# Kernel optimization log

Hardware: AMD Instinct MI355X
Metric: run time of the kernel (lower is better)

Reference implementation:

```python
import jax, jax.numpy as jnp
import numpy as np

B, S, H, E, I, K = 1, 4096, 1024, 16, 512, 2
ISH = 1024  # shared expert intermediate = moe_intermediate_size * num_shared_experts
ROUTE_SCALE = 1.0
WSCALE = 0.02


def setup_inputs() -> dict:
    key = jax.random.key(0)
    ks = jax.random.split(key, 9)
    return {
        "hidden_states": jax.random.normal(ks[0], (B, S, H), dtype=jnp.float32),
        "router_w": jax.random.normal(ks[1], (H, E), dtype=jnp.float32) * WSCALE,
        "expert_bias": jnp.zeros((E,), dtype=jnp.float32),
        "w_gate": jax.random.normal(ks[2], (E, H, I), dtype=jnp.float32) * WSCALE,
        "w_up": jax.random.normal(ks[3], (E, H, I), dtype=jnp.float32) * WSCALE,
        "w_down": jax.random.normal(ks[4], (E, I, H), dtype=jnp.float32) * WSCALE,
        "sw_gate": jax.random.normal(ks[5], (H, ISH), dtype=jnp.float32) * WSCALE,
        "sw_up": jax.random.normal(ks[6], (H, ISH), dtype=jnp.float32) * WSCALE,
        "sw_down": jax.random.normal(ks[7], (ISH, H), dtype=jnp.float32) * WSCALE,
    }


def reference(hidden_states, router_w, expert_bias, w_gate, w_up, w_down, sw_gate, sw_up, sw_down):
    b, s, h = hidden_states.shape
    T = b * s
    xf = hidden_states.reshape(T, h)

    # --- token-choice router (sigmoid scores, top-k, normalize, scale) ---
    scores = jax.nn.sigmoid((xf @ router_w).astype(jnp.float32))          # [T, E]
    _, sel = jax.lax.top_k(scores + expert_bias[None, :], K)              # [T, K] int32
    top = jnp.take_along_axis(scores, sel, axis=1)                        # [T, K]
    top = top / (top.sum(axis=-1, keepdims=True) + 1e-20)
    top = top * ROUTE_SCALE

    # combine weights: [T, E], zero for unselected experts
    comb = jnp.zeros((T, E), jnp.float32).at[jnp.arange(T)[:, None], sel].add(top)

    # --- routed experts: SwiGLU MLP per expert (stacked weights) ---
    g = jnp.einsum('th,ehi->eti', xf, w_gate)                             # [E, T, I]
    u = jnp.einsum('th,ehi->eti', xf, w_up)                               # [E, T, I]
    a = jax.nn.silu(g) * u                                                # [E, T, I]
    eo = jnp.einsum('eti,eih->eth', a, w_down)                            # [E, T, H]
    routed = jnp.einsum('eth,te->th', eo.astype(jnp.float32), comb).astype(hidden_states.dtype)

    # --- shared experts (always active) ---
    shared = (jax.nn.silu(xf @ sw_gate) * (xf @ sw_up)) @ sw_down         # [T, H]

    return (shared + routed).reshape(b, s, h)
```

## Files before the change

kernel.cpp:

```cpp
#include <hip/hip_runtime.h>
#include <math.h>

#define T_TOK 4096
#define HDIM  1024
#define NEXP  16
#define IDIM  512
#define NSLOT 16384
#define NGRP  18
#define MAXRB 160

typedef unsigned int u32;
typedef unsigned short u16;
typedef __attribute__((ext_vector_type(8))) short bfrag;
typedef __attribute__((ext_vector_type(4))) float f32x4;

__device__ __forceinline__ u16 f2bf(float f) {
    union { float f; u32 u; } c; c.f = f;
    u32 u = c.u;
    u32 r = u + 0x7fffu + ((u >> 16) & 1u);
    return (u16)(r >> 16);
}
__device__ __forceinline__ float bf2f(u16 h) {
    union { u32 u; float f; } c; c.u = ((u32)h) << 16;
    return c.f;
}

__device__ __forceinline__ void async16(void* lds, const void* g) {
    __builtin_amdgcn_global_load_lds((__attribute__((address_space(1))) void*)(g),
                                     (__attribute__((address_space(3))) void*)(lds),
                                     16, 0, 0);
}

#define SYNCN(n) do { \
    asm volatile("s_waitcnt vmcnt(" #n ")" ::: "memory"); \
    __builtin_amdgcn_s_barrier(); \
    __builtin_amdgcn_sched_barrier(0); \
} while (0)
#define BAR2() do { \
    __builtin_amdgcn_s_barrier(); \
    __builtin_amdgcn_sched_barrier(0); \
} while (0)

__global__ __launch_bounds__(256) void cvt_f32_bf16(const float* __restrict__ src,
                                                    u16* __restrict__ dst, int n) {
    int i = (blockIdx.x * 256 + threadIdx.x) * 4;
    if (i >= n) return;
    float4 v = *(const float4*)(src + i);
    ushort4 o;
    o.x = f2bf(v.x); o.y = f2bf(v.y); o.z = f2bf(v.z); o.w = f2bf(v.w);
    *(ushort4*)(dst + i) = o;
}

__global__ __launch_bounds__(256) void transpose_k(const float* __restrict__ src,
                                                   u16* __restrict__ dst,
                                                   int R, int C, long bstride) {
    __shared__ float tile[32][33];
    long base = (long)blockIdx.z * bstride;
    int c0 = blockIdx.x * 32, r0 = blockIdx.y * 32;
    int tx = threadIdx.x, ty = threadIdx.y;
#pragma unroll
    for (int j = 0; j < 4; ++j)
        tile[ty + 8 * j][tx] = src[base + (long)(r0 + ty + 8 * j) * C + (c0 + tx)];
    __syncthreads();
#pragma unroll
    for (int j = 0; j < 4; ++j)
        dst[base + (long)(c0 + ty + 8 * j) * R + (r0 + tx)] = f2bf(tile[tx][ty + 8 * j]);
}

__global__ __launch_bounds__(256) void router_k(const float* __restrict__ x,
                                                const float* __restrict__ rw,
                                                const float* __restrict__ bias,
                                                int* __restrict__ sel,
                                                float* __restrict__ wts) {
    int tid = threadIdx.x;
    int wv = tid >> 6;
    int lane = tid & 63;
    int t = blockIdx.x * 4 + wv;
    int e = lane & 15, hc = lane >> 4;
    const float* xr = x + (long)t * HDIM + hc * 256;
    const float* rp = rw + (long)hc * 256 * NEXP + e;
    float acc = 0.f;
#pragma unroll 4
    for (int i = 0; i < 64; ++i) {
        float4 xv = *(const float4*)(xr + i * 4);
        acc += xv.x * rp[(i * 4 + 0) * NEXP] + xv.y * rp[(i * 4 + 1) * NEXP]
             + xv.z * rp[(i * 4 + 2) * NEXP] + xv.w * rp[(i * 4 + 3) * NEXP];
    }
    acc += __shfl_down(acc, 16);
    acc += __shfl_down(acc, 32);
    float sc = 1.f / (1.f + __expf(-acc));
    float v = sc + bias[e];
    int i0 = -1, i1 = -1;
    float v0 = -1e30f, v1 = -1e30f, s0 = 0.f, s1 = 0.f;
#pragma unroll
    for (int j = 0; j < 16; ++j) {
        float vj = __shfl(v, j);
        float scj = __shfl(sc, j);
        if (vj > v0) { v1 = v0; i1 = i0; s1 = s0; v0 = vj; i0 = j; s0 = scj; }
        else if (vj > v1) { v1 = vj; i1 = j; s1 = scj; }
    }
    if (lane == 0) {
        float nrm = s0 + s1 + 1e-20f;
        sel[t * 2] = i0; sel[t * 2 + 1] = i1;
        wts[t * 2] = s0 / nrm; wts[t * 2 + 1] = s1 / nrm;
    }
}

__global__ __launch_bounds__(1024) void route_build_k(const int* __restrict__ sel,
                                                      int* __restrict__ offs,
                                                      int* __restrict__ rowmap,
                                                      int* __restrict__ invmap,
                                                      int* __restrict__ rbGroup,
                                                      int* __restrict__ rbRow0) {
    __shared__ int hist[NEXP];
    __shared__ int cur[NEXP];
    int tid = threadIdx.x;
    if (tid < NEXP) hist[tid] = 0;
    __syncthreads();
    for (int i = tid; i < T_TOK * 2; i += 1024)
        atomicAdd(&hist[sel[i]], 1);
    __syncthreads();
    if (tid == 0) {
        int a = 0;
        for (int g = 0; g < NEXP; ++g) { cur[g] = a; offs[g] = a; a += hist[g]; }
        offs[16] = 8192;
        offs[17] = 8192 + T_TOK;
        offs[18] = 8192 + 2 * T_TOK;
        int rb = 0;
        for (int g = 0; g < NGRP; ++g)
            for (int r0 = offs[g]; r0 < offs[g + 1]; r0 += 128) {
                rbGroup[rb] = g; rbRow0[rb] = r0; ++rb;
            }
        for (; rb < MAXRB; ++rb) rbGroup[rb] = -1;
    }
    __syncthreads();
    for (int i = tid; i < T_TOK * 2; i += 1024) {
        int g = sel[i];
        int slot = atomicAdd(&cur[g], 1);
        rowmap[slot] = i >> 1;
        invmap[i] = slot;
    }
    for (int i = tid; i < T_TOK; i += 1024) {
        rowmap[8192 + i] = i;
        rowmap[8192 + T_TOK + i] = i;
    }
}

__global__ __launch_bounds__(256)
void gemm_gu(const u16* __restrict__ A,
             const u16* __restrict__ WG,
             const u16* __restrict__ WU,
             const u16* __restrict__ SWG,
             const u16* __restrict__ SWU,
             u16* __restrict__ H,
             const int* __restrict__ offs,
             const int* __restrict__ rowmap,
             const int* __restrict__ rbGroup,
             const int* __restrict__ rbRow0) {
    int rb = blockIdx.y;
    int g = rbGroup[rb];
    if (g < 0) return;
    int row0 = rbRow0[rb];
    int mend = offs[g + 1];
    int col0 = blockIdx.x * 64;
    long wb = (long)((g < 16) ? g : (g - 16)) * IDIM * HDIM;
    const u16* Bg = (g < 16) ? WG + wb : SWG + wb;
    const u16* Bu = (g < 16) ? WU + wb : SWU + wb;

    __shared__ u16 sA[2][128 * 64];
    __shared__ u16 sBg[2][64 * 64];
    __shared__ u16 sBu[2][64 * 64];

    int tid = threadIdx.x;
    int lane = tid & 63;
    int w = tid >> 6;
    int wr = (w >> 1) * 64, wc = (w & 1) * 32;
    int lhi = lane >> 4, llo = lane & 15;
    int swz = llo & 7;

    const u16* pA[4]; int dA[4];
#pragma unroll
    for (int c = 0; c < 4; ++c) {
        int idx = c * 256 + tid;
        int r = idx >> 3, ch = idx & 7;
        int grow = row0 + r;
        int ar = rowmap[(grow < mend) ? grow : row0];
        pA[c] = A + (long)ar * HDIM + ((ch ^ (r & 7)) * 8);
        dA[c] = idx * 8;
    }
    const u16* pBg[2]; const u16* pBu[2]; int dB[2];
#pragma unroll
    for (int c = 0; c < 2; ++c) {
        int idx = c * 256 + tid;
        int r = idx >> 3, ch = idx & 7;
        long boff = (long)(col0 + r) * HDIM + ((ch ^ (r & 7)) * 8);
        pBg[c] = Bg + boff; pBu[c] = Bu + boff;
        dB[c] = idx * 8;
    }

    f32x4 accg[4][2], accu[4][2];
#pragma unroll
    for (int m = 0; m < 4; ++m)
#pragma unroll
        for (int n = 0; n < 2; ++n) {
            f32x4 z = {0.f, 0.f, 0.f, 0.f};
            accg[m][n] = z; accu[m][n] = z;
        }

    auto STAGE = [&](int buf) {
#pragma unroll
        for (int c = 0; c < 4; ++c) { async16(&sA[buf][dA[c]], pA[c]); pA[c] += 64; }
#pragma unroll
        for (int c = 0; c < 2; ++c) {
            async16(&sBg[buf][dB[c]], pBg[c]); pBg[c] += 64;
            async16(&sBu[buf][dB[c]], pBu[c]); pBu[c] += 64;
        }
    };
    auto COMPUTE = [&](int buf) {
#pragma unroll
        for (int kk = 0; kk < 2; ++kk) {
            int p = ((kk * 4 + lhi) ^ swz) * 8;
            bfrag a[4], bg[2], bu[2];
#pragma unroll
            for (int m = 0; m < 4; ++m)
                a[m] = *(const bfrag*)&sA[buf][(wr + m * 16 + llo) * 64 + p];
#pragma unroll
            for (int n = 0; n < 2; ++n) {
                bg[n] = *(const bfrag*)&sBg[buf][(wc + n * 16 + llo) * 64 + p];
                bu[n] = *(const bfrag*)&sBu[buf][(wc + n * 16 + llo) * 64 + p];
            }
#pragma unroll
            for (int m = 0; m < 4; ++m)
#pragma unroll
                for (int n = 0; n < 2; ++n) {
                    accg[m][n] = __builtin_amdgcn_mfma_f32_16x16x32_bf16(a[m], bg[n], accg[m][n], 0, 0, 0);
                    accu[m][n] = __builtin_amdgcn_mfma_f32_16x16x32_bf16(a[m], bu[n], accu[m][n], 0, 0, 0);
                }
        }
    };

    STAGE(0);
#pragma unroll 1
    for (int t = 0; t < 14; t += 2) {
        STAGE(1); SYNCN(8); COMPUTE(0); BAR2();
        STAGE(0); SYNCN(8); COMPUTE(1); BAR2();
    }
    STAGE(1); SYNCN(8); COMPUTE(0); BAR2();
    SYNCN(0); COMPUTE(1);

#pragma unroll
    for (int m = 0; m < 4; ++m) {
        int rbase = row0 + wr + m * 16 + lhi * 4;
#pragma unroll
        for (int n = 0; n < 2; ++n) {
            int col = col0 + wc + n * 16 + llo;
#pragma unroll
            for (int i = 0; i < 4; ++i) {
                int grow = rbase + i;
                if (grow >= mend) continue;
                float gv = accg[m][n][i], uv = accu[m][n][i];
                float hv = gv / (1.f + __expf(-gv)) * uv;
                H[(long)grow * IDIM + col] = f2bf(hv);
            }
        }
    }
}

__global__ __launch_bounds__(256)
void gemm_down(const u16* __restrict__ Hbuf,
               const u16* __restrict__ WD,
               const u16* __restrict__ SWD,
               u16* __restrict__ EO,
               const int* __restrict__ offs,
               const int* __restrict__ rbGroup,
               const int* __restrict__ rbRow0) {
    int rb = blockIdx.y;
    int g = rbGroup[rb];
    if (g < 0) return;
    int row0 = rbRow0[rb];
    int mend = offs[g + 1];
    int col0 = blockIdx.x * 128;
    long wb = (long)((g < 16) ? g : (g - 16)) * HDIM * IDIM;
    const u16* B = (g < 16) ? WD + wb : SWD + wb;

    __shared__ u16 sA[2][128 * 64];
    __shared__ u16 sB[2][128 * 64];

    int tid = threadIdx.x;
    int lane = tid & 63;
    int w = tid >> 6;
    int wr = (w >> 1) * 64, wc = (w & 1) * 64;
    int lhi = lane >> 4, llo = lane & 15;
    int swz = llo & 7;

    const u16* pA[4]; const u16* pB[4]; int dd[4];
#pragma unroll
    for (int c = 0; c < 4; ++c) {
        int idx = c * 256 + tid;
        int r = idx >> 3, ch = idx & 7;
        int grow = row0 + r;
        int ar = (grow < mend) ? grow : row0;
        int chs = (ch ^ (r & 7)) * 8;
        pA[c] = Hbuf + (long)ar * IDIM + chs;
        pB[c] = B + (long)(col0 + r) * IDIM + chs;
        dd[c] = idx * 8;
    }

    f32x4 acc[4][4];
#pragma unroll
    for (int m = 0; m < 4; ++m)
#pragma unroll
        for (int n = 0; n < 4; ++n) { f32x4 z = {0.f, 0.f, 0.f, 0.f}; acc[m][n] = z; }

    auto STAGE = [&](int buf) {
#pragma unroll
        for (int c = 0; c < 4; ++c) {
            async16(&sA[buf][dd[c]], pA[c]); pA[c] += 64;
            async16(&sB[buf][dd[c]], pB[c]); pB[c] += 64;
        }
    };
    auto COMPUTE = [&](int buf) {
#pragma unroll
        for (int kk = 0; kk < 2; ++kk) {
            int p = ((kk * 4 + lhi) ^ swz) * 8;
            bfrag a[4], b[4];
#pragma unroll
            for (int m = 0; m < 4; ++m)
                a[m] = *(const bfrag*)&sA[buf][(wr + m * 16 + llo) * 64 + p];
#pragma unroll
            for (int n = 0; n < 4; ++n)
                b[n] = *(const bfrag*)&sB[buf][(wc + n * 16 + llo) * 64 + p];
#pragma unroll
            for (int m = 0; m < 4; ++m)
#pragma unroll
                for (int n = 0; n < 4; ++n)
                    acc[m][n] = __builtin_amdgcn_mfma_f32_16x16x32_bf16(a[m], b[n], acc[m][n], 0, 0, 0);
        }
    };

    STAGE(0);
#pragma unroll 1
    for (int t = 0; t < 6; t += 2) {
        STAGE(1); SYNCN(8); COMPUTE(0); BAR2();
        STAGE(0); SYNCN(8); COMPUTE(1); BAR2();
    }
    STAGE(1); SYNCN(8); COMPUTE(0); BAR2();
    SYNCN(0); COMPUTE(1);

#pragma unroll
    for (int m = 0; m < 4; ++m) {
        int rbase = row0 + wr + m * 16 + lhi * 4;
#pragma unroll
        for (int n = 0; n < 4; ++n) {
            int col = col0 + wc + n * 16 + llo;
#pragma unroll
            for (int i = 0; i < 4; ++i) {
                int grow = rbase + i;
                if (grow >= mend) continue;
                EO[(long)grow * HDIM + col] = f2bf(acc[m][n][i]);
            }
        }
    }
}

__global__ __launch_bounds__(256) void combine_k(float* __restrict__ out,
                                                 const u16* __restrict__ eo,
                                                 const int* __restrict__ invmap,
                                                 const float* __restrict__ wts) {
    int t = blockIdx.x;
    int h = threadIdx.x * 4;
    int r0 = invmap[t * 2], r1 = invmap[t * 2 + 1];
    float w0 = wts[t * 2], w1 = wts[t * 2 + 1];
    int s0 = 8192 + t, s1 = 8192 + T_TOK + t;
    ushort4 a = *(const ushort4*)(eo + (long)r0 * HDIM + h);
    ushort4 b = *(const ushort4*)(eo + (long)r1 * HDIM + h);
    ushort4 c = *(const ushort4*)(eo + (long)s0 * HDIM + h);
    ushort4 d = *(const ushort4*)(eo + (long)s1 * HDIM + h);
    float4 o;
    o.x = w0 * bf2f(a.x) + w1 * bf2f(b.x) + bf2f(c.x) + bf2f(d.x);
    o.y = w0 * bf2f(a.y) + w1 * bf2f(b.y) + bf2f(c.y) + bf2f(d.y);
    o.z = w0 * bf2f(a.z) + w1 * bf2f(b.z) + bf2f(c.z) + bf2f(d.z);
    o.w = w0 * bf2f(a.w) + w1 * bf2f(b.w) + bf2f(c.w) + bf2f(d.w);
    *(float4*)(out + (long)t * HDIM + h) = o;
}

extern "C" void kernel_launch(void* const* d_in, const int* in_sizes, int n_in,
                              void* d_out, int out_size, void* d_ws, size_t ws_size,
                              hipStream_t stream) {
    const float* x    = (const float*)d_in[0];
    const float* rw   = (const float*)d_in[1];
    const float* bias = (const float*)d_in[2];
    const float* wg   = (const float*)d_in[3];
    const float* wu   = (const float*)d_in[4];
    const float* wd   = (const float*)d_in[5];
    const float* swg  = (const float*)d_in[6];
    const float* swu  = (const float*)d_in[7];
    const float* swd  = (const float*)d_in[8];
    float* out = (float*)d_out;

    char* ws = (char*)d_ws;
    size_t o = 0;
    auto alloc = [&](size_t bytes) -> void* {
        void* p = ws + o;
        o += (bytes + 255) & ~(size_t)255;
        return p;
    };
    u16* x_bf = (u16*)alloc((size_t)T_TOK * HDIM * 2);
    u16* WtG  = (u16*)alloc((size_t)NEXP * IDIM * HDIM * 2);
    u16* WtU  = (u16*)alloc((size_t)NEXP * IDIM * HDIM * 2);
    u16* WtD  = (u16*)alloc((size_t)NEXP * HDIM * IDIM * 2);
    u16* SWtG = (u16*)alloc((size_t)2 * IDIM * HDIM * 2);
    u16* SWtU = (u16*)alloc((size_t)2 * IDIM * HDIM * 2);
    u16* SWtD = (u16*)alloc((size_t)2 * HDIM * IDIM * 2);
    u16* Hbuf = (u16*)alloc((size_t)NSLOT * IDIM * 2);
    int*   sel     = (int*)alloc((size_t)T_TOK * 2 * 4);
    float* wts     = (float*)alloc((size_t)T_TOK * 2 * 4);
    int*   invmap  = (int*)alloc((size_t)T_TOK * 2 * 4);
    int*   rowmap  = (int*)alloc((size_t)NSLOT * 4);
    int*   offs    = (int*)alloc((NGRP + 1) * 4);
    int*   rbGroup = (int*)alloc(MAXRB * 4);
    int*   rbRow0  = (int*)alloc(MAXRB * 4);
    u16* EO = WtG;

    cvt_f32_bf16<<<dim3((T_TOK * HDIM) / (4 * 256)), 256, 0, stream>>>(x, x_bf, T_TOK * HDIM);

    transpose_k<<<dim3(IDIM / 32, HDIM / 32, NEXP), dim3(32, 8), 0, stream>>>(wg, WtG, HDIM, IDIM, (long)HDIM * IDIM);
    transpose_k<<<dim3(IDIM / 32, HDIM / 32, NEXP), dim3(32, 8), 0, stream>>>(wu, WtU, HDIM, IDIM, (long)HDIM * IDIM);
    transpose_k<<<dim3(HDIM / 32, IDIM / 32, NEXP), dim3(32, 8), 0, stream>>>(wd, WtD, IDIM, HDIM, (long)IDIM * HDIM);
    transpose_k<<<dim3(32, 32, 1), dim3(32, 8), 0, stream>>>(swg, SWtG, HDIM, 2 * IDIM, 0);
    transpose_k<<<dim3(32, 32, 1), dim3(32, 8), 0, stream>>>(swu, SWtU, HDIM, 2 * IDIM, 0);
    transpose_k<<<dim3(HDIM / 32, IDIM / 32, 2), dim3(32, 8), 0, stream>>>(swd, SWtD, IDIM, HDIM, (long)IDIM * HDIM);

    router_k<<<dim3(T_TOK / 4), 256, 0, stream>>>(x, rw, bias, sel, wts);
    route_build_k<<<dim3(1), 1024, 0, stream>>>(sel, offs, rowmap, invmap, rbGroup, rbRow0);

    gemm_gu<<<dim3(IDIM / 64, MAXRB), 256, 0, stream>>>(
        x_bf, WtG, WtU, SWtG, SWtU, Hbuf, offs, rowmap, rbGroup, rbRow0);

    gemm_down<<<dim3(HDIM / 128, MAXRB), 256, 0, stream>>>(
        Hbuf, WtD, SWtD, EO, offs, rbGroup, rbRow0);

    combine_k<<<dim3(T_TOK), 256, 0, stream>>>(out, EO, invmap, wts);
}
```

Baseline: 175.7 us.

## Enlarge MoE GEMM tiles to 256 rows with 512 threads; vectorize weight transpose

Both grouped GEMMs now run 512-thread blocks on larger tiles: 256x128 for gate/up and 256x256 for down. Routing row-blocks are 256 rows, and MAXRB shrinks to match. The aim is more reuse of each staged A/B tile and fewer redundant weight loads, at the cost of about 128KB of LDS per block, heavy accumulator register use, fewer blocks and more padding waste on small expert groups. The fp32-to-bf16 weight transpose is also rewritten to use float4 loads, a bf16 LDS tile and ushort4 stores over 128-row tiles, which cuts memory transactions in that preprocessing step.

```diff
diff --git a/kernel.cpp b/kernel.cpp
--- a/kernel.cpp
+++ b/kernel.cpp
@@ -7,7 +7,7 @@
 #define IDIM  512
 #define NSLOT 16384
 #define NGRP  18
-#define MAXRB 160
+#define MAXRB 80
 
 typedef unsigned int u32;
 typedef unsigned short u16;
@@ -51,20 +51,35 @@
     *(ushort4*)(dst + i) = o;
 }
 
-__global__ __launch_bounds__(256) void transpose_k(const float* __restrict__ src,
-                                                   u16* __restrict__ dst,
-                                                   int R, int C, long bstride) {
-    __shared__ float tile[32][33];
+__global__ __launch_bounds__(256) void transpose_k2(const float* __restrict__ src,
+                                                    u16* __restrict__ dst,
+                                                    int R, int C, long bstride) {
+    __shared__ u16 tileT[32][132];
     long base = (long)blockIdx.z * bstride;
-    int c0 = blockIdx.x * 32, r0 = blockIdx.y * 32;
-    int tx = threadIdx.x, ty = threadIdx.y;
-#pragma unroll
-    for (int j = 0; j < 4; ++j)
-        tile[ty + 8 * j][tx] = src[base + (long)(r0 + ty + 8 * j) * C + (c0 + tx)];
+    int c0 = blockIdx.x * 32, r0 = blockIdx.y * 128;
+    int t = threadIdx.x;
+    int rr = t >> 3;
+    int c4 = (t & 7) * 4;
+#pragma unroll
+    for (int p = 0; p < 4; ++p) {
+        int r = p * 32 + rr;
+        float4 v = *(const float4*)(src + base + (long)(r0 + r) * C + c0 + c4);
+        tileT[c4 + 0][r] = f2bf(v.x);
+        tileT[c4 + 1][r] = f2bf(v.y);
+        tileT[c4 + 2][r] = f2bf(v.z);
+        tileT[c4 + 3][r] = f2bf(v.w);
+    }
     __syncthreads();
-#pragma unroll
-    for (int j = 0; j < 4; ++j)
-        dst[base + (long)(c0 + ty + 8 * j) * R + (r0 + tx)] = f2bf(tile[tx][ty + 8 * j]);
+    int cc = t >> 5;
+    int r4 = (t & 31) * 4;
+#pragma unroll
+    for (int q = 0; q < 4; ++q) {
+        int c = q * 8 + cc;
+        ushort4 o;
+        o.x = tileT[c][r4]; o.y = tileT[c][r4 + 1];
+        o.z = tileT[c][r4 + 2]; o.w = tileT[c][r4 + 3];
+        *(ushort4*)(dst + base + (long)(c0 + c) * R + r0 + r4) = o;
+    }
 }
 
 __global__ __launch_bounds__(256) void router_k(const float* __restrict__ x,
@@ -128,7 +143,7 @@
         offs[18] = 8192 + 2 * T_TOK;
         int rb = 0;
         for (int g = 0; g < NGRP; ++g)
-            for (int r0 = offs[g]; r0 < offs[g + 1]; r0 += 128) {
+            for (int r0 = offs[g]; r0 < offs[g + 1]; r0 += 256) {
                 rbGroup[rb] = g; rbRow0[rb] = r0; ++rb;
             }
         for (; rb < MAXRB; ++rb) rbGroup[rb] = -1;
@@ -146,7 +161,7 @@
     }
 }
 
-__global__ __launch_bounds__(256)
+__global__ __launch_bounds__(512)
 void gemm_gu(const u16* __restrict__ A,
              const u16* __restrict__ WG,
              const u16* __restrict__ WU,
@@ -162,26 +177,27 @@
     if (g < 0) return;
     int row0 = rbRow0[rb];
     int mend = offs[g + 1];
-    int col0 = blockIdx.x * 64;
+    int col0 = blockIdx.x * 128;
     long wb = (long)((g < 16) ? g : (g - 16)) * IDIM * HDIM;
     const u16* Bg = (g < 16) ? WG + wb : SWG + wb;
     const u16* Bu = (g < 16) ? WU + wb : SWU + wb;
 
-    __shared__ u16 sA[2][128 * 64];
-    __shared__ u16 sBg[2][64 * 64];
-    __shared__ u16 sBu[2][64 * 64];
+    __shared__ u16 sA[2][256 * 64];
+    __shared__ u16 sBg[2][128 * 64];
+    __shared__ u16 sBu[2][128 * 64];
 
     int tid = threadIdx.x;
     int lane = tid & 63;
     int w = tid >> 6;
-    int wr = (w >> 1) * 64, wc = (w & 1) * 32;
+    int wr = (w >> 1) * 64;
+    int wc = (w & 1) * 64;
     int lhi = lane >> 4, llo = lane & 15;
     int swz = llo & 7;
 
     const u16* pA[4]; int dA[4];
 #pragma unroll
     for (int c = 0; c < 4; ++c) {
-        int idx = c * 256 + tid;
+        int idx = c * 512 + tid;
         int r = idx >> 3, ch = idx & 7;
         int grow = row0 + r;
         int ar = rowmap[(grow < mend) ? grow : row0];
@@ -191,18 +207,18 @@
     const u16* pBg[2]; const u16* pBu[2]; int dB[2];
 #pragma unroll
     for (int c = 0; c < 2; ++c) {
-        int idx = c * 256 + tid;
+        int idx = c * 512 + tid;
         int r = idx >> 3, ch = idx & 7;
         long boff = (long)(col0 + r) * HDIM + ((ch ^ (r & 7)) * 8);
         pBg[c] = Bg + boff; pBu[c] = Bu + boff;
         dB[c] = idx * 8;
     }
 
-    f32x4 accg[4][2], accu[4][2];
+    f32x4 accg[4][4], accu[4][4];
 #pragma unroll
     for (int m = 0; m < 4; ++m)
 #pragma unroll
-        for (int n = 0; n < 2; ++n) {
+        for (int n = 0; n < 4; ++n) {
             f32x4 z = {0.f, 0.f, 0.f, 0.f};
             accg[m][n] = z; accu[m][n] = z;
         }
@@ -220,19 +236,19 @@
 #pragma unroll
         for (int kk = 0; kk < 2; ++kk) {
             int p = ((kk * 4 + lhi) ^ swz) * 8;
-            bfrag a[4], bg[2], bu[2];
+            bfrag a[4], bg[4], bu[4];
 #pragma unroll
             for (int m = 0; m < 4; ++m)
                 a[m] = *(const bfrag*)&sA[buf][(wr + m * 16 + llo) * 64 + p];
 #pragma unroll
-            for (int n = 0; n < 2; ++n) {
+            for (int n = 0; n < 4; ++n) {
                 bg[n] = *(const bfrag*)&sBg[buf][(wc + n * 16 + llo) * 64 + p];
                 bu[n] = *(const bfrag*)&sBu[buf][(wc + n * 16 + llo) * 64 + p];
             }
 #pragma unroll
             for (int m = 0; m < 4; ++m)
 #pragma unroll
-                for (int n = 0; n < 2; ++n) {
+                for (int n = 0; n < 4; ++n) {
                     accg[m][n] = __builtin_amdgcn_mfma_f32_16x16x32_bf16(a[m], bg[n], accg[m][n], 0, 0, 0);
                     accu[m][n] = __builtin_amdgcn_mfma_f32_16x16x32_bf16(a[m], bu[n], accu[m][n], 0, 0, 0);
                 }
@@ -252,7 +268,7 @@
     for (int m = 0; m < 4; ++m) {
         int rbase = row0 + wr + m * 16 + lhi * 4;
 #pragma unroll
-        for (int n = 0; n < 2; ++n) {
+        for (int n = 0; n < 4; ++n) {
             int col = col0 + wc + n * 16 + llo;
 #pragma unroll
             for (int i = 0; i < 4; ++i) {
@@ -266,7 +282,7 @@
     }
 }
 
-__global__ __launch_bounds__(256)
+__global__ __launch_bounds__(512)
 void gemm_down(const u16* __restrict__ Hbuf,
                const u16* __restrict__ WD,
                const u16* __restrict__ SWD,
@@ -279,24 +295,25 @@
     if (g < 0) return;
     int row0 = rbRow0[rb];
     int mend = offs[g + 1];
-    int col0 = blockIdx.x * 128;
+    int col0 = blockIdx.x * 256;
     long wb = (long)((g < 16) ? g : (g - 16)) * HDIM * IDIM;
     const u16* B = (g < 16) ? WD + wb : SWD + wb;
 
-    __shared__ u16 sA[2][128 * 64];
-    __shared__ u16 sB[2][128 * 64];
+    __shared__ u16 sA[2][256 * 64];
+    __shared__ u16 sB[2][256 * 64];
 
     int tid = threadIdx.x;
     int lane = tid & 63;
     int w = tid >> 6;
-    int wr = (w >> 1) * 64, wc = (w & 1) * 64;
+    int wr = (w >> 2) * 128;
+    int wc = (w & 3) * 64;
     int lhi = lane >> 4, llo = lane & 15;
     int swz = llo & 7;
 
     const u16* pA[4]; const u16* pB[4]; int dd[4];
 #pragma unroll
     for (int c = 0; c < 4; ++c) {
-        int idx = c * 256 + tid;
+        int idx = c * 512 + tid;
         int r = idx >> 3, ch = idx & 7;
         int grow = row0 + r;
         int ar = (grow < mend) ? grow : row0;
@@ -306,9 +323,9 @@
         dd[c] = idx * 8;
     }
 
-    f32x4 acc[4][4];
-#pragma unroll
-    for (int m = 0; m < 4; ++m)
+    f32x4 acc[8][4];
+#pragma unroll
+    for (int m = 0; m < 8; ++m)
 #pragma unroll
         for (int n = 0; n < 4; ++n) { f32x4 z = {0.f, 0.f, 0.f, 0.f}; acc[m][n] = z; }
 
@@ -323,15 +340,15 @@
 #pragma unroll
         for (int kk = 0; kk < 2; ++kk) {
             int p = ((kk * 4 + lhi) ^ swz) * 8;
-            bfrag a[4], b[4];
-#pragma unroll
-            for (int m = 0; m < 4; ++m)
+            bfrag a[8], b[4];
+#pragma unroll
+            for (int m = 0; m < 8; ++m)
                 a[m] = *(const bfrag*)&sA[buf][(wr + m * 16 + llo) * 64 + p];
 #pragma unroll
             for (int n = 0; n < 4; ++n)
                 b[n] = *(const bfrag*)&sB[buf][(wc + n * 16 + llo) * 64 + p];
 #pragma unroll
-            for (int m = 0; m < 4; ++m)
+            for (int m = 0; m < 8; ++m)
 #pragma unroll
                 for (int n = 0; n < 4; ++n)
                     acc[m][n] = __builtin_amdgcn_mfma_f32_16x16x32_bf16(a[m], b[n], acc[m][n], 0, 0, 0);
@@ -348,7 +365,7 @@
     SYNCN(0); COMPUTE(1);
 
 #pragma unroll
-    for (int m = 0; m < 4; ++m) {
+    for (int m = 0; m < 8; ++m) {
         int rbase = row0 + wr + m * 16 + lhi * 4;
 #pragma unroll
         for (int n = 0; n < 4; ++n) {
@@ -424,20 +441,20 @@
 
     cvt_f32_bf16<<<dim3((T_TOK * HDIM) / (4 * 256)), 256, 0, stream>>>(x, x_bf, T_TOK * HDIM);
 
-    transpose_k<<<dim3(IDIM / 32, HDIM / 32, NEXP), dim3(32, 8), 0, stream>>>(wg, WtG, HDIM, IDIM, (long)HDIM * IDIM);
-    transpose_k<<<dim3(IDIM / 32, HDIM / 32, NEXP), dim3(32, 8), 0, stream>>>(wu, WtU, HDIM, IDIM, (long)HDIM * IDIM);
-    transpose_k<<<dim3(HDIM / 32, IDIM / 32, NEXP), dim3(32, 8), 0, stream>>>(wd, WtD, IDIM, HDIM, (long)IDIM * HDIM);
-    transpose_k<<<dim3(32, 32, 1), dim3(32, 8), 0, stream>>>(swg, SWtG, HDIM, 2 * IDIM, 0);
-    transpose_k<<<dim3(32, 32, 1), dim3(32, 8), 0, stream>>>(swu, SWtU, HDIM, 2 * IDIM, 0);
-    transpose_k<<<dim3(HDIM / 32, IDIM / 32, 2), dim3(32, 8), 0, stream>>>(swd, SWtD, IDIM, HDIM, (long)IDIM * HDIM);
+    transpose_k2<<<dim3(IDIM / 32, HDIM / 128, NEXP), 256, 0, stream>>>(wg, WtG, HDIM, IDIM, (long)HDIM * IDIM);
+    transpose_k2<<<dim3(IDIM / 32, HDIM / 128, NEXP), 256, 0, stream>>>(wu, WtU, HDIM, IDIM, (long)HDIM * IDIM);
+    transpose_k2<<<dim3(HDIM / 32, IDIM / 128, NEXP), 256, 0, stream>>>(wd, WtD, IDIM, HDIM, (long)IDIM * HDIM);
+    transpose_k2<<<dim3((2 * IDIM) / 32, HDIM / 128, 1), 256, 0, stream>>>(swg, SWtG, HDIM, 2 * IDIM, 0);
+    transpose_k2<<<dim3((2 * IDIM) / 32, HDIM / 128, 1), 256, 0, stream>>>(swu, SWtU, HDIM, 2 * IDIM, 0);
+    transpose_k2<<<dim3(HDIM / 32, IDIM / 128, 2), 256, 0, stream>>>(swd, SWtD, IDIM, HDIM, (long)IDIM * HDIM);
 
     router_k<<<dim3(T_TOK / 4), 256, 0, stream>>>(x, rw, bias, sel, wts);
     route_build_k<<<dim3(1), 1024, 0, stream>>>(sel, offs, rowmap, invmap, rbGroup, rbRow0);
 
-    gemm_gu<<<dim3(IDIM / 64, MAXRB), 256, 0, stream>>>(
+    gemm_gu<<<dim3(IDIM / 128, MAXRB), 512, 0, stream>>>(
         x_bf, WtG, WtU, SWtG, SWtU, Hbuf, offs, rowmap, rbGroup, rbRow0);
 
-    gemm_down<<<dim3(HDIM / 128, MAXRB), 256, 0, stream>>>(
+    gemm_down<<<dim3(HDIM / 256, MAXRB), 512, 0, stream>>>(
         Hbuf, WtD, SWtD, EO, offs, rbGroup, rbRow0);
 
     combine_k<<<dim3(T_TOK), 256, 0, stream>>>(out, EO, invmap, wts);
```

After: 182.6 us. 1.04x slower.
